# Kernel optimization log

Measured on AMD Instinct MI355X. Metric: run time of the kernel, lower is better.

The kernel has to match this reference:

```python
import jax, jax.numpy as jnp
import numpy as np

N_INT4, N_INT8, K, GROUP = 6144, 2048, 8192, 128
N_TOTAL = N_INT4 + N_INT8
M = 16


def setup_inputs() -> dict:
    key = jax.random.key(0)
    ks = jax.random.split(key, 8)
    x = jax.random.normal(ks[0], (M, K), jnp.float32)
    # uint4 weights: values 0..15 (stored int32)
    w_int4 = jax.random.randint(ks[1], (N_INT4, K), 0, 16, jnp.int32)
    # group-wise scales [N_int4, K//group_size]
    s_int4 = jax.random.uniform(ks[2], (N_INT4, K // GROUP), jnp.float32, minval=0.005, maxval=0.02)
    # int8 weights stored in offset-128 form (w_int8 + 128 -> 0..255), as pack_for_marlin builds
    w_uint8 = jax.random.randint(ks[3], (N_INT8, K), 0, 256, jnp.int32)
    # per-channel int8 scales
    s_int8 = jax.random.uniform(ks[4], (N_INT8,), jnp.float32, minval=0.005, maxval=0.02)
    awq_scales = jax.random.uniform(ks[5], (K,), jnp.float32, minval=0.5, maxval=2.0)
    bias = jax.random.normal(ks[6], (N_TOTAL,), jnp.float32) * 0.01
    inv_perm = jax.random.permutation(ks[7], N_TOTAL).astype(jnp.int32)
    return dict(x=x, w_int4=w_int4, s_int4=s_int4, w_uint8=w_uint8, s_int8=s_int8,
                awq_scales=awq_scales, bias=bias, inv_perm=inv_perm, group_size=GROUP)


def reference(x, w_int4, s_int4, w_uint8, s_int8, awq_scales, bias, inv_perm, group_size):
    dt = x.dtype
    k = x.shape[-1]
    # AWQ input scaling (unfused path: x / awq_scales)
    x2 = x.reshape(-1, k) / awq_scales[None, :]
    sum_x = jnp.sum(x2, axis=1, keepdims=True)  # [M, 1]

    # Marlin uint4b8 dequant: (q - 8) * scale, group-wise scales for int4 rows
    s4_k = jnp.repeat(s_int4, group_size, axis=1)            # [N4, K]
    W4 = (w_int4.astype(dt) - 8.0) * s4_k                    # [N4, K]

    # int8 rows split into high/low nibbles with scales 16*s and s
    high = (w_uint8 >> 4) & 15
    low = w_uint8 & 15
    Wh = (high.astype(dt) - 8.0) * (16.0 * s_int8)[:, None]  # [N8, K]
    Wl = (low.astype(dt) - 8.0) * s_int8[:, None]            # [N8, K]

    Wc = jnp.concatenate([W4, Wh, Wl], axis=0)               # [N4+2*N8, K]
    y = x2 @ Wc.T                                            # marlin_gemm equivalent

    n4 = W4.shape[0]
    n8 = s_int8.shape[0]
    y4 = y[:, :n4]
    # int8 reconstruction: y_high + y_low + 8*s_int8*sum_x  == s_int8 * (x @ w_int8^T)
    y8 = y[:, n4:n4 + n8] + y[:, n4 + n8:] + (8.0 * s_int8)[None, :] * sum_x
    y_out = jnp.concatenate([y4, y8], axis=-1)[:, inv_perm] + bias[None, :]
    return y_out.reshape(*x.shape[:-1], n4 + n8)
```

## Files before the change

### kernel.cpp

```cpp
#include <hip/hip_runtime.h>

constexpr int K    = 8192;
constexpr int N4   = 6144;
constexpr int N8   = 2048;
constexpr int NT   = N4 + N8;
constexpr int NG   = K / 128;
constexpr int SPLIT = 4;
constexpr int KS    = K / SPLIT;
constexpr int ITERS = KS / 256;

__global__ void prep_kernel(const float* __restrict__ x,
                            const float* __restrict__ awq,
                            const int*   __restrict__ inv_perm,
                            const float* __restrict__ bias,
                            float* __restrict__ x2,
                            int*   __restrict__ fwd,
                            float* __restrict__ out) {
    const int tid = blockIdx.x * blockDim.x + threadIdx.x;
    x2[tid]  = x[tid] / awq[tid & (K - 1)];
    out[tid] = bias[tid & (NT - 1)];
    if (tid < NT) fwd[inv_perm[tid]] = tid;
}

__global__ __launch_bounds__(256)
void qgemv_kernel(const float* __restrict__ x2,
                  const int*   __restrict__ w4,
                  const float* __restrict__ s4,
                  const int*   __restrict__ w8,
                  const float* __restrict__ s8,
                  const int*   __restrict__ fwd,
                  float* __restrict__ out) {
    __shared__ float lds[4 * 1040];
    float* tile = lds;

    const int t    = threadIdx.x;
    const int lane = t & 63;
    const int w    = t >> 6;
    const int nblk = blockIdx.x & 511;
    const int spl  = blockIdx.x >> 9;
    const int nb   = nblk * 16 + w * 4;
    const int kb   = spl * KS;

    float acc[4][16];
    #pragma unroll
    for (int r = 0; r < 4; ++r)
        #pragma unroll
        for (int m = 0; m < 16; ++m) acc[r][m] = 0.f;

    const bool is4 = (nb < N4);
    const int* wr  = is4 ? (w4 + (size_t)nb * K) : (w8 + (size_t)(nb - N4) * K);

    #pragma unroll 1
    for (int it = 0; it < ITERS; ++it) {
        const int k0 = kb + it * 256;

        #pragma unroll
        for (int q = 0; q < 4; ++q) {
            const int m = q * 4 + w;
            const float4 v = *(const float4*)(x2 + (size_t)m * K + k0 + lane * 4);
            *(float4*)(tile + m * 256 + lane * 4) = v;
        }
        __syncthreads();

        const int kl = k0 + lane * 4;
        float wf[4][4];
        if (is4) {
            const int g = spl * (KS / 128) + it * 2 + (lane >> 5);
            #pragma unroll
            for (int r = 0; r < 4; ++r) {
                const int4 wv = *(const int4*)(wr + (size_t)r * K + kl);
                const float s   = s4[(nb + r) * NG + g];
                const float m8s = -8.f * s;
                wf[r][0] = (float)wv.x * s + m8s;
                wf[r][1] = (float)wv.y * s + m8s;
                wf[r][2] = (float)wv.z * s + m8s;
                wf[r][3] = (float)wv.w * s + m8s;
            }
        } else {
            #pragma unroll
            for (int r = 0; r < 4; ++r) {
                const int4 wv = *(const int4*)(wr + (size_t)r * K + kl);
                wf[r][0] = (float)wv.x - 128.f;
                wf[r][1] = (float)wv.y - 128.f;
                wf[r][2] = (float)wv.z - 128.f;
                wf[r][3] = (float)wv.w - 128.f;
            }
        }

        #pragma unroll
        for (int m = 0; m < 16; ++m) {
            const float4 xv = *(const float4*)(tile + m * 256 + lane * 4);
            #pragma unroll
            for (int r = 0; r < 4; ++r) {
                acc[r][m] += xv.x * wf[r][0] + xv.y * wf[r][1]
                           + xv.z * wf[r][2] + xv.w * wf[r][3];
            }
        }
        __syncthreads();
    }

    float* red = lds + w * 1040;
    #pragma unroll
    for (int r = 0; r < 4; ++r) {
        __syncthreads();
        #pragma unroll
        for (int m = 0; m < 16; ++m) red[m * 65 + lane] = acc[r][m];
        __syncthreads();

        const int m = lane & 15;
        const int q = lane >> 4;
        float p = 0.f;
        #pragma unroll
        for (int j = 0; j < 16; ++j) p += red[m * 65 + q * 16 + j];
        p += __shfl_xor(p, 16, 64);
        p += __shfl_xor(p, 32, 64);

        if (lane < 16) {
            const int n = nb + r;
            float v = p;
            if (n >= N4) v *= s8[n - N4];
            unsafeAtomicAdd(&out[(size_t)lane * NT + fwd[n]], v);
        }
    }
}

extern "C" void kernel_launch(void* const* d_in, const int* in_sizes, int n_in,
                              void* d_out, int out_size, void* d_ws, size_t ws_size,
                              hipStream_t stream) {
    const float* x        = (const float*)d_in[0];
    const int*   w_int4   = (const int*)  d_in[1];
    const float* s_int4   = (const float*)d_in[2];
    const int*   w_uint8  = (const int*)  d_in[3];
    const float* s_int8   = (const float*)d_in[4];
    const float* awq      = (const float*)d_in[5];
    const float* bias     = (const float*)d_in[6];
    const int*   inv_perm = (const int*)  d_in[7];

    float* x2  = (float*)d_ws;
    int*   fwd = (int*)((char*)d_ws + (size_t)16 * K * sizeof(float));

    prep_kernel<<<(16 * K) / 256, 256, 0, stream>>>(x, awq, inv_perm, bias,
                                                    x2, fwd, (float*)d_out);
    qgemv_kernel<<<512 * SPLIT, 256, 0, stream>>>(x2, w_int4, s_int4,
                                                  w_uint8, s_int8, fwd,
                                                  (float*)d_out);
}
```

Baseline: 339.5 us.

## Replace FP32 FMA GEMV with bf16 MFMA 16x16x32 and pre-swizzled activations

The scalar FP32 dot-product loop, with its LDS tiling and cross-lane reduction, becomes bf16 MFMA instructions. Each wavefront computes a 16-row by 16-column tile over a K slice with 16-way split-K. The prep kernel now writes the scaled activations as bf16 already laid out in MFMA A-fragment order. Weights are dequantised in registers to bf16 and fed as B fragments. This removes LDS traffic, barriers and most ALU work, but adds bf16 rounding error and four times as many atomic adds.

```diff
diff --git a/kernel.cpp b/kernel.cpp
--- a/kernel.cpp
+++ b/kernel.cpp
@@ -1,126 +1,100 @@
 #include <hip/hip_runtime.h>
+#include <hip/hip_bf16.h>
 
 constexpr int K    = 8192;
 constexpr int N4   = 6144;
 constexpr int N8   = 2048;
 constexpr int NT   = N4 + N8;
 constexpr int NG   = K / 128;
-constexpr int SPLIT = 4;
-constexpr int KS    = K / SPLIT;
-constexpr int ITERS = KS / 256;
+constexpr int SPLITS = 16;
+constexpr int CPS    = 16;
+
+typedef short  short8  __attribute__((ext_vector_type(8)));
+typedef float  floatx4 __attribute__((ext_vector_type(4)));
+
+__device__ inline short f2bf(float f) {
+    __hip_bfloat16 h = __float2bfloat16(f);
+    return __builtin_bit_cast(short, h);
+}
 
 __global__ void prep_kernel(const float* __restrict__ x,
                             const float* __restrict__ awq,
                             const int*   __restrict__ inv_perm,
                             const float* __restrict__ bias,
-                            float* __restrict__ x2,
+                            short* __restrict__ x2bf,
                             int*   __restrict__ fwd,
                             float* __restrict__ out) {
-    const int tid = blockIdx.x * blockDim.x + threadIdx.x;
-    x2[tid]  = x[tid] / awq[tid & (K - 1)];
-    out[tid] = bias[tid & (NT - 1)];
+    const int tid  = blockIdx.x * blockDim.x + threadIdx.x;
+    const int c    = tid >> 9;
+    const int rem  = tid & 511;
+    const int lane = rem >> 3;
+    const int j    = rem & 7;
+    const int m    = lane & 15;
+    const int k    = c * 32 + (lane >> 4) * 8 + j;
+    x2bf[tid] = f2bf(x[m * K + k] / awq[k]);
+    out[tid]  = bias[tid & (NT - 1)];
     if (tid < NT) fwd[inv_perm[tid]] = tid;
 }
 
 __global__ __launch_bounds__(256)
-void qgemv_kernel(const float* __restrict__ x2,
+void qgemv_kernel(const short* __restrict__ xf,
                   const int*   __restrict__ w4,
                   const float* __restrict__ s4,
                   const int*   __restrict__ w8,
                   const float* __restrict__ s8,
                   const int*   __restrict__ fwd,
                   float* __restrict__ out) {
-    __shared__ float lds[4 * 1040];
-    float* tile = lds;
-
     const int t    = threadIdx.x;
     const int lane = t & 63;
-    const int w    = t >> 6;
-    const int nblk = blockIdx.x & 511;
-    const int spl  = blockIdx.x >> 9;
-    const int nb   = nblk * 16 + w * 4;
-    const int kb   = spl * KS;
-
-    float acc[4][16];
-    #pragma unroll
-    for (int r = 0; r < 4; ++r)
-        #pragma unroll
-        for (int m = 0; m < 16; ++m) acc[r][m] = 0.f;
+    const int wid  = blockIdx.x * 4 + (t >> 6);
+    const int tile = wid >> 4;
+    const int spl  = wid & (SPLITS - 1);
+    const int nb   = tile * 16;
+    const int i    = lane & 15;
+    const int q    = lane >> 4;
+    const int row  = nb + i;
 
     const bool is4 = (nb < N4);
-    const int* wr  = is4 ? (w4 + (size_t)nb * K) : (w8 + (size_t)(nb - N4) * K);
+    const int* wr  = is4 ? (w4 + (size_t)row * K + q * 8)
+                         : (w8 + (size_t)(row - N4) * K + q * 8);
+    const int c0   = spl * CPS;
+
+    floatx4 acc = {0.f, 0.f, 0.f, 0.f};
 
     #pragma unroll 1
-    for (int it = 0; it < ITERS; ++it) {
-        const int k0 = kb + it * 256;
+    for (int gi = 0; gi < 4; ++gi) {
+        const int g   = (c0 >> 2) + gi;
+        const float s  = is4 ? s4[row * NG + g] : 1.f;
+        const float sb = is4 ? -8.f * s : -128.f;
 
         #pragma unroll
-        for (int q = 0; q < 4; ++q) {
-            const int m = q * 4 + w;
-            const float4 v = *(const float4*)(x2 + (size_t)m * K + k0 + lane * 4);
-            *(float4*)(tile + m * 256 + lane * 4) = v;
+        for (int ci = 0; ci < 4; ++ci) {
+            const int c = c0 + gi * 4 + ci;
+            const int4 wa = *(const int4*)(wr + (size_t)c * 32);
+            const int4 wb = *(const int4*)(wr + (size_t)c * 32 + 4);
+
+            short8 bfrag;
+            bfrag[0] = f2bf((float)wa.x * s + sb);
+            bfrag[1] = f2bf((float)wa.y * s + sb);
+            bfrag[2] = f2bf((float)wa.z * s + sb);
+            bfrag[3] = f2bf((float)wa.w * s + sb);
+            bfrag[4] = f2bf((float)wb.x * s + sb);
+            bfrag[5] = f2bf((float)wb.y * s + sb);
+            bfrag[6] = f2bf((float)wb.z * s + sb);
+            bfrag[7] = f2bf((float)wb.w * s + sb);
+
+            const short8 afrag = *(const short8*)(xf + (size_t)c * 512 + lane * 8);
+
+            acc = __builtin_amdgcn_mfma_f32_16x16x32_bf16(afrag, bfrag, acc, 0, 0, 0);
         }
-        __syncthreads();
-
-        const int kl = k0 + lane * 4;
-        float wf[4][4];
-        if (is4) {
-            const int g = spl * (KS / 128) + it * 2 + (lane >> 5);
-            #pragma unroll
-            for (int r = 0; r < 4; ++r) {
-                const int4 wv = *(const int4*)(wr + (size_t)r * K + kl);
-                const float s   = s4[(nb + r) * NG + g];
-                const float m8s = -8.f * s;
-                wf[r][0] = (float)wv.x * s + m8s;
-                wf[r][1] = (float)wv.y * s + m8s;
-                wf[r][2] = (float)wv.z * s + m8s;
-                wf[r][3] = (float)wv.w * s + m8s;
-            }
-        } else {
-            #pragma unroll
-            for (int r = 0; r < 4; ++r) {
-                const int4 wv = *(const int4*)(wr + (size_t)r * K + kl);
-                wf[r][0] = (float)wv.x - 128.f;
-                wf[r][1] = (float)wv.y - 128.f;
-                wf[r][2] = (float)wv.z - 128.f;
-                wf[r][3] = (float)wv.w - 128.f;
-            }
-        }
-
-        #pragma unroll
-        for (int m = 0; m < 16; ++m) {
-            const float4 xv = *(const float4*)(tile + m * 256 + lane * 4);
-            #pragma unroll
-            for (int r = 0; r < 4; ++r) {
-                acc[r][m] += xv.x * wf[r][0] + xv.y * wf[r][1]
-                           + xv.z * wf[r][2] + xv.w * wf[r][3];
-            }
-        }
-        __syncthreads();
     }
 
-    float* red = lds + w * 1040;
+    const float sc = is4 ? 1.f : s8[row - N4];
+    const int   d  = fwd[row];
     #pragma unroll
     for (int r = 0; r < 4; ++r) {
-        __syncthreads();
-        #pragma unroll
-        for (int m = 0; m < 16; ++m) red[m * 65 + lane] = acc[r][m];
-        __syncthreads();
-
-        const int m = lane & 15;
-        const int q = lane >> 4;
-        float p = 0.f;
-        #pragma unroll
-        for (int j = 0; j < 16; ++j) p += red[m * 65 + q * 16 + j];
-        p += __shfl_xor(p, 16, 64);
-        p += __shfl_xor(p, 32, 64);
-
-        if (lane < 16) {
-            const int n = nb + r;
-            float v = p;
-            if (n >= N4) v *= s8[n - N4];
-            unsafeAtomicAdd(&out[(size_t)lane * NT + fwd[n]], v);
-        }
+        const int m = q * 4 + r;
+        unsafeAtomicAdd(&out[(size_t)m * NT + d], acc[r] * sc);
     }
 }
 
@@ -136,12 +110,12 @@
     const float* bias     = (const float*)d_in[6];
     const int*   inv_perm = (const int*)  d_in[7];
 
-    float* x2  = (float*)d_ws;
-    int*   fwd = (int*)((char*)d_ws + (size_t)16 * K * sizeof(float));
+    short* x2bf = (short*)d_ws;
+    int*   fwd  = (int*)((char*)d_ws + (size_t)16 * K * sizeof(short));
 
     prep_kernel<<<(16 * K) / 256, 256, 0, stream>>>(x, awq, inv_perm, bias,
-                                                    x2, fwd, (float*)d_out);
-    qgemv_kernel<<<512 * SPLIT, 256, 0, stream>>>(x2, w_int4, s_int4,
-                                                  w_uint8, s_int8, fwd,
-                                                  (float*)d_out);
+                                                    x2bf, fwd, (float*)d_out);
+    qgemv_kernel<<<2048, 256, 0, stream>>>(x2bf, w_int4, s_int4,
+                                           w_uint8, s_int8, fwd,
+                                           (float*)d_out);
 }
```

Measured after the change: 370.5 us. +9.1%, slower.
